# Performance work log

Measured on AMD Instinct MI355X. Metric: run time of the kernel, lower is better.

## Reference

```python
import jax, jax.numpy as jnp
import numpy as np

N_NODES = 100_000
N_EDGES = 1_600_000
F_DIM = 32


def setup_inputs() -> dict:
    key = jax.random.key(0)
    k1, k2, k3 = jax.random.split(key, 3)
    x = jax.random.normal(k1, (N_NODES, F_DIM), dtype=jnp.float32)
    edge_index = jax.random.randint(k2, (2, N_EDGES), 0, N_NODES, dtype=jnp.int64)
    edge_weight = jax.random.uniform(k3, (N_EDGES,), dtype=jnp.float32)
    w_mp = jnp.array([0.5], dtype=jnp.float32)  # learned scalar parameter
    return {"x": x, "edge_index": edge_index, "edge_weight": edge_weight, "w_mp": w_mp}


def reference(x, edge_index, edge_weight, w_mp):
    # message: ea = w_mp * x[src] * edge_weight  (shape [E, F])
    # aggregate: sum messages into target nodes (aggr='add', source_to_target)
    src = edge_index[0]
    dst = edge_index[1]
    ea = (w_mp * x[src]) * edge_weight[:, None]          # [E, F]
    out = jax.ops.segment_sum(ea, dst, num_segments=x.shape[0])  # [N, F]
    return out
```

## Files before the change

kernel.cpp:

```cpp
#include <hip/hip_runtime.h>


constexpr int N_NODES = 100000;
constexpr int N_EDGES = 1600000;
constexpr int F_DIM   = 32;

constexpr int NPB_C = 256;
constexpr int NB_C  = (N_NODES + NPB_C - 1) / NPB_C;
constexpr int CAP_C = 4608;

constexpr int CUR_STRIDE = 32;

constexpr int BIN_THREADS = 1024;
constexpr int BIN_BLOCKS  = 512;
constexpr int BIN_CHUNK   = N_EDGES / BIN_BLOCKS;
constexpr int BIN_EPT     = (BIN_CHUNK + BIN_THREADS - 1) / BIN_THREADS;

constexpr int AGG_THREADS = 1024;
constexpr int GRPT = (CAP_C + AGG_THREADS - 1) / AGG_THREADS;

constexpr size_t WS_CURSOR  = 0;
constexpr size_t WS_RECORDS = 64 * 1024;
constexpr size_t WS_NEEDED  = WS_RECORDS + (size_t)NB_C * CAP_C * 8;

__global__ __launch_bounds__(BIN_THREADS, 8) void bin_edges(
    const int* __restrict__ src, const int* __restrict__ dst,
    const float* __restrict__ ew, const float* __restrict__ w_mp,
    int* __restrict__ gcursor, uint2* __restrict__ records)
{
    __shared__ uint2 srt[BIN_CHUNK];
    __shared__ unsigned short srtb[BIN_CHUNK];
    __shared__ int lhist[NB_C];
    __shared__ int loff[NB_C];
    __shared__ int lbase[NB_C];
    __shared__ int lcur[NB_C];
    __shared__ int wsum[8];
    __shared__ int wexc[8];

    const int t    = threadIdx.x;
    const int lane = t & 63;
    const int wv   = t >> 6;

    if (t < NB_C) lhist[t] = 0;
    __syncthreads();

    const float w = w_mp[0];
    const int e0    = blockIdx.x * BIN_CHUNK;
    const int e_end = min(e0 + BIN_CHUNK, N_EDGES);
    const int cnt   = e_end - e0;

    int   bkt[BIN_EPT];
    uint2 rec[BIN_EPT];
    #pragma unroll
    for (int i = 0; i < BIN_EPT; ++i) {
        int j = t + i * BIN_THREADS;
        bkt[i] = -1;
        if (j < cnt) {
            int e = e0 + j;
            int d = dst[e];
            int b = d >> 8;
            bkt[i] = b;
            rec[i].x = __float_as_uint(w * ew[e]);
            rec[i].y = (unsigned)src[e] | ((unsigned)(d & 255) << 24);
            atomicAdd(&lhist[b], 1);
        }
    }
    __syncthreads();

    if (t < 448) {
        int v = (t < NB_C) ? lhist[t] : 0;
        int inc = v;
        #pragma unroll
        for (int d = 1; d < 64; d <<= 1) {
            int o = __shfl_up(inc, d, 64);
            if (lane >= d) inc += o;
        }
        if (lane == 63) wsum[wv] = inc;
        if (t < NB_C) loff[t] = inc - v;
    }
    __syncthreads();
    if (t < 64) {
        int v = (t < 7) ? wsum[t] : 0;
        int inc = v;
        #pragma unroll
        for (int d = 1; d < 8; d <<= 1) {
            int o = __shfl_up(inc, d, 64);
            if (t >= d) inc += o;
        }
        if (t < 7) wexc[t] = inc - v;
    }
    __syncthreads();

    if (t < NB_C) {
        int off = loff[t] + wexc[t >> 6];
        loff[t] = off;
        int c = lhist[t];
        int base = c ? atomicAdd(&gcursor[t * CUR_STRIDE], c) : 0;
        lbase[t] = t * CAP_C + base - off;
        lcur[t]  = off;
    }
    __syncthreads();

    #pragma unroll
    for (int i = 0; i < BIN_EPT; ++i) {
        if (bkt[i] >= 0) {
            int s = atomicAdd(&lcur[bkt[i]], 1);
            srt[s]  = rec[i];
            srtb[s] = (unsigned short)bkt[i];
        }
    }
    __syncthreads();

    for (int j = t; j < cnt; j += BIN_THREADS) {
        int b   = srtb[j];
        int pos = lbase[b] + j;
        if (pos < (b + 1) * CAP_C)
            records[pos] = srt[j];
    }
}

__global__ __launch_bounds__(AGG_THREADS, 8) void sort_gather(
    const int*   __restrict__ gcursor,
    const uint2* __restrict__ records,
    const float* __restrict__ x,
    float*       __restrict__ out)
{
    __shared__ uint2 sorted[CAP_C];
    __shared__ int   hist[NPB_C];
    __shared__ int   offs[NPB_C + 1];
    __shared__ int   cursor[NPB_C];

    const int coarse = blockIdx.x;
    const int t      = threadIdx.x;

    if (t < NPB_C) hist[t] = 0;
    __syncthreads();

    const int rbase = coarse * CAP_C;
    const int cnt   = min(gcursor[coarse * CUR_STRIDE], CAP_C);

    uint2 rec[GRPT];
    #pragma unroll
    for (int i = 0; i < GRPT; ++i) {
        int j = t + i * AGG_THREADS;
        rec[i].y = 0xFFFFFFFFu;
        if (j < cnt) {
            rec[i] = records[rbase + j];
            atomicAdd(&hist[rec[i].y >> 24], 1);
        }
    }
    __syncthreads();

    if (t < 64) {
        const int b4 = t * 4;
        int h0 = hist[b4], h1 = hist[b4 + 1], h2 = hist[b4 + 2], h3 = hist[b4 + 3];
        int s   = h0 + h1 + h2 + h3;
        int inc = s;
        #pragma unroll
        for (int d = 1; d < 64; d <<= 1) {
            int o = __shfl_up(inc, d, 64);
            if (t >= d) inc += o;
        }
        int base = inc - s;
        offs[b4]     = base;
        offs[b4 + 1] = base + h0;
        offs[b4 + 2] = base + h0 + h1;
        offs[b4 + 3] = base + h0 + h1 + h2;
        cursor[b4]     = base;
        cursor[b4 + 1] = base + h0;
        cursor[b4 + 2] = base + h0 + h1;
        cursor[b4 + 3] = base + h0 + h1 + h2;
        if (t == 63) offs[NPB_C] = inc;
    }
    __syncthreads();

    #pragma unroll
    for (int i = 0; i < GRPT; ++i) {
        if (rec[i].y != 0xFFFFFFFFu) {
            int slot = atomicAdd(&cursor[rec[i].y >> 24], 1);
            sorted[slot] = rec[i];
        }
    }
    __syncthreads();

    const int qq = (t & 7) * 4;
    #pragma unroll
    for (int p = 0; p < 2; ++p) {
        const int node  = p * (AGG_THREADS / 8) + (t >> 3);
        const int gnode = coarse * NPB_C + node;
        if (gnode >= N_NODES) continue;

        int j  = offs[node];
        int je = offs[node + 1];
        float4 acc = make_float4(0.f, 0.f, 0.f, 0.f);

        for (; j + 4 <= je; j += 4) {
            uint2 r0 = sorted[j + 0];
            uint2 r1 = sorted[j + 1];
            uint2 r2 = sorted[j + 2];
            uint2 r3 = sorted[j + 3];
            const float4 v0 = *reinterpret_cast<const float4*>(
                x + (size_t)(r0.y & 0xFFFFFFu) * F_DIM + qq);
            const float4 v1 = *reinterpret_cast<const float4*>(
                x + (size_t)(r1.y & 0xFFFFFFu) * F_DIM + qq);
            const float4 v2 = *reinterpret_cast<const float4*>(
                x + (size_t)(r2.y & 0xFFFFFFu) * F_DIM + qq);
            const float4 v3 = *reinterpret_cast<const float4*>(
                x + (size_t)(r3.y & 0xFFFFFFu) * F_DIM + qq);
            float c0 = __uint_as_float(r0.x), c1 = __uint_as_float(r1.x);
            float c2 = __uint_as_float(r2.x), c3 = __uint_as_float(r3.x);
            acc.x += c0 * v0.x + c1 * v1.x + c2 * v2.x + c3 * v3.x;
            acc.y += c0 * v0.y + c1 * v1.y + c2 * v2.y + c3 * v3.y;
            acc.z += c0 * v0.z + c1 * v1.z + c2 * v2.z + c3 * v3.z;
            acc.w += c0 * v0.w + c1 * v1.w + c2 * v2.w + c3 * v3.w;
        }
        for (; j < je; ++j) {
            uint2 r = sorted[j];
            float c = __uint_as_float(r.x);
            const float4 v = *reinterpret_cast<const float4*>(
                x + (size_t)(r.y & 0xFFFFFFu) * F_DIM + qq);
            acc.x += c * v.x;
            acc.y += c * v.y;
            acc.z += c * v.z;
            acc.w += c * v.w;
        }
        *reinterpret_cast<float4*>(out + (size_t)gnode * F_DIM + qq) = acc;
    }
}

__global__ __launch_bounds__(256) void gnn_scatter_atomic(
    const float* __restrict__ x, const int* __restrict__ src,
    const int* __restrict__ dst, const float* __restrict__ ew,
    const float* __restrict__ w_mp, float* __restrict__ out)
{
    const float w = w_mp[0];
    int gid = blockIdx.x * blockDim.x + threadIdx.x;
    int e = gid >> 3;
    int qq = (gid & 7) * 4;
    if (e >= N_EDGES) return;
    int s = src[e];
    int d = dst[e];
    float c = w * ew[e];
    const float4 xv = *reinterpret_cast<const float4*>(x + (size_t)s * F_DIM + qq);
    float* op = out + (size_t)d * F_DIM + qq;
    atomicAdd(op + 0, c * xv.x);
    atomicAdd(op + 1, c * xv.y);
    atomicAdd(op + 2, c * xv.z);
    atomicAdd(op + 3, c * xv.w);
}

extern "C" void kernel_launch(void* const* d_in, const int* in_sizes, int n_in,
                              void* d_out, int out_size, void* d_ws, size_t ws_size,
                              hipStream_t stream) {
    const float* x    = (const float*)d_in[0];
    const int*   ei   = (const int*)d_in[1];
    const float* ew   = (const float*)d_in[2];
    const float* w_mp = (const float*)d_in[3];
    float* out = (float*)d_out;

    const int* src = ei;
    const int* dst = ei + N_EDGES;

    if (ws_size < WS_NEEDED) {
        hipMemsetAsync(d_out, 0, (size_t)out_size * sizeof(float), stream);
        int total = N_EDGES * 8;
        gnn_scatter_atomic<<<(total + 255) / 256, 256, 0, stream>>>(
            x, src, dst, ew, w_mp, out);
        return;
    }

    char* ws = (char*)d_ws;
    int*   gcursor = (int*)(ws + WS_CURSOR);
    uint2* records = (uint2*)(ws + WS_RECORDS);

    hipMemsetAsync(gcursor, 0, NB_C * CUR_STRIDE * sizeof(int), stream);
    bin_edges<<<BIN_BLOCKS, BIN_THREADS, 0, stream>>>(src, dst, ew, w_mp,
                                                      gcursor, records);
    sort_gather<<<NB_C, AGG_THREADS, 0, stream>>>(gcursor, records, x, out);
}
```

Baseline: 122.4 us.

## Fuse binning and sort-gather into one persistent kernel with grid barrier

Merges the edge-binning kernel and the per-bucket sort/gather kernel into a single persistent kernel of 256 blocks. A software grid barrier on a global atomic counter separates the two phases, and shared memory is reused through a union. The aim is to remove one kernel launch and the idle gap between the kernels. In exchange, the number of blocks falls from 512 and 391 to 256, so each phase has less parallelism, and the barrier needs all 256 blocks to be co-resident or it can deadlock.

```diff
diff --git a/kernel.cpp b/kernel.cpp
--- a/kernel.cpp
+++ b/kernel.cpp
@@ -11,220 +11,236 @@
 
 constexpr int CUR_STRIDE = 32;
 
-constexpr int BIN_THREADS = 1024;
-constexpr int BIN_BLOCKS  = 512;
-constexpr int BIN_CHUNK   = N_EDGES / BIN_BLOCKS;
-constexpr int BIN_EPT     = (BIN_CHUNK + BIN_THREADS - 1) / BIN_THREADS;
-
-constexpr int AGG_THREADS = 1024;
-constexpr int GRPT = (CAP_C + AGG_THREADS - 1) / AGG_THREADS;
-
-constexpr size_t WS_CURSOR  = 0;
+constexpr int THREADS = 1024;
+constexpr int GRID    = 256;
+constexpr int NSUB    = 2;
+constexpr int SUBCH   = N_EDGES / (GRID * NSUB);
+constexpr int EPT     = (SUBCH + THREADS - 1) / THREADS;
+constexpr int GRPT    = (CAP_C + THREADS - 1) / THREADS;
+
+constexpr size_t WS_BAR     = 0;
+constexpr size_t WS_CURSOR  = 128;
 constexpr size_t WS_RECORDS = 64 * 1024;
 constexpr size_t WS_NEEDED  = WS_RECORDS + (size_t)NB_C * CAP_C * 8;
-
-__global__ __launch_bounds__(BIN_THREADS, 8) void bin_edges(
+constexpr size_t WS_ZERO    = 128 + (size_t)NB_C * CUR_STRIDE * 4;
+
+struct P1 {
+    uint2 srt[SUBCH];
+    unsigned short srtb[SUBCH];
+    int lhist[NB_C];
+    int loff[NB_C];
+    int lbase[NB_C];
+    int lcur[NB_C];
+    int wsum[8];
+    int wexc[8];
+};
+struct P2s {
+    uint2 sorted[CAP_C];
+    int hist[NPB_C];
+    int offs[NPB_C + 1];
+    int cursor[NPB_C];
+};
+union Smem { P1 p1; P2s p2; };
+
+__global__ __launch_bounds__(THREADS, 4) void fused_gnn(
     const int* __restrict__ src, const int* __restrict__ dst,
     const float* __restrict__ ew, const float* __restrict__ w_mp,
-    int* __restrict__ gcursor, uint2* __restrict__ records)
+    int* __restrict__ bar, int* __restrict__ gcursor,
+    uint2* __restrict__ records,
+    const float* __restrict__ x, float* __restrict__ out)
 {
-    __shared__ uint2 srt[BIN_CHUNK];
-    __shared__ unsigned short srtb[BIN_CHUNK];
-    __shared__ int lhist[NB_C];
-    __shared__ int loff[NB_C];
-    __shared__ int lbase[NB_C];
-    __shared__ int lcur[NB_C];
-    __shared__ int wsum[8];
-    __shared__ int wexc[8];
-
+    __shared__ Smem sm;
     const int t    = threadIdx.x;
     const int lane = t & 63;
     const int wv   = t >> 6;
-
-    if (t < NB_C) lhist[t] = 0;
+    const float w  = w_mp[0];
+
+    for (int sc = 0; sc < NSUB; ++sc) {
+        P1& p = sm.p1;
+        __syncthreads();
+        if (t < NB_C) p.lhist[t] = 0;
+        __syncthreads();
+
+        const int e0 = (blockIdx.x * NSUB + sc) * SUBCH;
+
+        int   bkt[EPT];
+        uint2 rec[EPT];
+        #pragma unroll
+        for (int i = 0; i < EPT; ++i) {
+            int j = t + i * THREADS;
+            bkt[i] = -1;
+            if (j < SUBCH) {
+                int e = e0 + j;
+                int d = dst[e];
+                int b = d >> 8;
+                bkt[i] = b;
+                rec[i].x = __float_as_uint(w * ew[e]);
+                rec[i].y = (unsigned)src[e] | ((unsigned)(d & 255) << 24);
+                atomicAdd(&p.lhist[b], 1);
+            }
+        }
+        __syncthreads();
+
+        if (t < 448) {
+            int v = (t < NB_C) ? p.lhist[t] : 0;
+            int inc = v;
+            #pragma unroll
+            for (int d = 1; d < 64; d <<= 1) {
+                int o = __shfl_up(inc, d, 64);
+                if (lane >= d) inc += o;
+            }
+            if (lane == 63) p.wsum[wv] = inc;
+            if (t < NB_C) p.loff[t] = inc - v;
+        }
+        __syncthreads();
+        if (t < 64) {
+            int v = (t < 7) ? p.wsum[t] : 0;
+            int inc = v;
+            #pragma unroll
+            for (int d = 1; d < 8; d <<= 1) {
+                int o = __shfl_up(inc, d, 64);
+                if (t >= d) inc += o;
+            }
+            if (t < 7) p.wexc[t] = inc - v;
+        }
+        __syncthreads();
+
+        if (t < NB_C) {
+            int off = p.loff[t] + p.wexc[t >> 6];
+            int c   = p.lhist[t];
+            int base = c ? atomicAdd(&gcursor[t * CUR_STRIDE], c) : 0;
+            p.lbase[t] = t * CAP_C + base - off;
+            p.lcur[t]  = off;
+        }
+        __syncthreads();
+
+        #pragma unroll
+        for (int i = 0; i < EPT; ++i) {
+            if (bkt[i] >= 0) {
+                int s = atomicAdd(&p.lcur[bkt[i]], 1);
+                p.srt[s]  = rec[i];
+                p.srtb[s] = (unsigned short)bkt[i];
+            }
+        }
+        __syncthreads();
+
+        for (int j = t; j < SUBCH; j += THREADS) {
+            int b   = p.srtb[j];
+            int pos = p.lbase[b] + j;
+            if (pos < (b + 1) * CAP_C)
+                records[pos] = p.srt[j];
+        }
+    }
+
+    __threadfence();
     __syncthreads();
-
-    const float w = w_mp[0];
-    const int e0    = blockIdx.x * BIN_CHUNK;
-    const int e_end = min(e0 + BIN_CHUNK, N_EDGES);
-    const int cnt   = e_end - e0;
-
-    int   bkt[BIN_EPT];
-    uint2 rec[BIN_EPT];
-    #pragma unroll
-    for (int i = 0; i < BIN_EPT; ++i) {
-        int j = t + i * BIN_THREADS;
-        bkt[i] = -1;
-        if (j < cnt) {
-            int e = e0 + j;
-            int d = dst[e];
-            int b = d >> 8;
-            bkt[i] = b;
-            rec[i].x = __float_as_uint(w * ew[e]);
-            rec[i].y = (unsigned)src[e] | ((unsigned)(d & 255) << 24);
-            atomicAdd(&lhist[b], 1);
-        }
+    if (t == 0) {
+        __hip_atomic_fetch_add(bar, 1, __ATOMIC_ACQ_REL,
+                               __HIP_MEMORY_SCOPE_AGENT);
+        while (__hip_atomic_load(bar, __ATOMIC_ACQUIRE,
+                                 __HIP_MEMORY_SCOPE_AGENT) < GRID)
+            __builtin_amdgcn_s_sleep(2);
     }
     __syncthreads();
-
-    if (t < 448) {
-        int v = (t < NB_C) ? lhist[t] : 0;
-        int inc = v;
-        #pragma unroll
-        for (int d = 1; d < 64; d <<= 1) {
-            int o = __shfl_up(inc, d, 64);
-            if (lane >= d) inc += o;
-        }
-        if (lane == 63) wsum[wv] = inc;
-        if (t < NB_C) loff[t] = inc - v;
-    }
-    __syncthreads();
-    if (t < 64) {
-        int v = (t < 7) ? wsum[t] : 0;
-        int inc = v;
-        #pragma unroll
-        for (int d = 1; d < 8; d <<= 1) {
-            int o = __shfl_up(inc, d, 64);
-            if (t >= d) inc += o;
-        }
-        if (t < 7) wexc[t] = inc - v;
-    }
-    __syncthreads();
-
-    if (t < NB_C) {
-        int off = loff[t] + wexc[t >> 6];
-        loff[t] = off;
-        int c = lhist[t];
-        int base = c ? atomicAdd(&gcursor[t * CUR_STRIDE], c) : 0;
-        lbase[t] = t * CAP_C + base - off;
-        lcur[t]  = off;
-    }
-    __syncthreads();
-
-    #pragma unroll
-    for (int i = 0; i < BIN_EPT; ++i) {
-        if (bkt[i] >= 0) {
-            int s = atomicAdd(&lcur[bkt[i]], 1);
-            srt[s]  = rec[i];
-            srtb[s] = (unsigned short)bkt[i];
-        }
-    }
-    __syncthreads();
-
-    for (int j = t; j < cnt; j += BIN_THREADS) {
-        int b   = srtb[j];
-        int pos = lbase[b] + j;
-        if (pos < (b + 1) * CAP_C)
-            records[pos] = srt[j];
-    }
-}
-
-__global__ __launch_bounds__(AGG_THREADS, 8) void sort_gather(
-    const int*   __restrict__ gcursor,
-    const uint2* __restrict__ records,
-    const float* __restrict__ x,
-    float*       __restrict__ out)
-{
-    __shared__ uint2 sorted[CAP_C];
-    __shared__ int   hist[NPB_C];
-    __shared__ int   offs[NPB_C + 1];
-    __shared__ int   cursor[NPB_C];
-
-    const int coarse = blockIdx.x;
-    const int t      = threadIdx.x;
-
-    if (t < NPB_C) hist[t] = 0;
-    __syncthreads();
-
-    const int rbase = coarse * CAP_C;
-    const int cnt   = min(gcursor[coarse * CUR_STRIDE], CAP_C);
-
-    uint2 rec[GRPT];
-    #pragma unroll
-    for (int i = 0; i < GRPT; ++i) {
-        int j = t + i * AGG_THREADS;
-        rec[i].y = 0xFFFFFFFFu;
-        if (j < cnt) {
-            rec[i] = records[rbase + j];
-            atomicAdd(&hist[rec[i].y >> 24], 1);
-        }
-    }
-    __syncthreads();
-
-    if (t < 64) {
-        const int b4 = t * 4;
-        int h0 = hist[b4], h1 = hist[b4 + 1], h2 = hist[b4 + 2], h3 = hist[b4 + 3];
-        int s   = h0 + h1 + h2 + h3;
-        int inc = s;
-        #pragma unroll
-        for (int d = 1; d < 64; d <<= 1) {
-            int o = __shfl_up(inc, d, 64);
-            if (t >= d) inc += o;
-        }
-        int base = inc - s;
-        offs[b4]     = base;
-        offs[b4 + 1] = base + h0;
-        offs[b4 + 2] = base + h0 + h1;
-        offs[b4 + 3] = base + h0 + h1 + h2;
-        cursor[b4]     = base;
-        cursor[b4 + 1] = base + h0;
-        cursor[b4 + 2] = base + h0 + h1;
-        cursor[b4 + 3] = base + h0 + h1 + h2;
-        if (t == 63) offs[NPB_C] = inc;
-    }
-    __syncthreads();
-
-    #pragma unroll
-    for (int i = 0; i < GRPT; ++i) {
-        if (rec[i].y != 0xFFFFFFFFu) {
-            int slot = atomicAdd(&cursor[rec[i].y >> 24], 1);
-            sorted[slot] = rec[i];
-        }
-    }
-    __syncthreads();
-
-    const int qq = (t & 7) * 4;
-    #pragma unroll
-    for (int p = 0; p < 2; ++p) {
-        const int node  = p * (AGG_THREADS / 8) + (t >> 3);
-        const int gnode = coarse * NPB_C + node;
-        if (gnode >= N_NODES) continue;
-
-        int j  = offs[node];
-        int je = offs[node + 1];
-        float4 acc = make_float4(0.f, 0.f, 0.f, 0.f);
-
-        for (; j + 4 <= je; j += 4) {
-            uint2 r0 = sorted[j + 0];
-            uint2 r1 = sorted[j + 1];
-            uint2 r2 = sorted[j + 2];
-            uint2 r3 = sorted[j + 3];
-            const float4 v0 = *reinterpret_cast<const float4*>(
-                x + (size_t)(r0.y & 0xFFFFFFu) * F_DIM + qq);
-            const float4 v1 = *reinterpret_cast<const float4*>(
-                x + (size_t)(r1.y & 0xFFFFFFu) * F_DIM + qq);
-            const float4 v2 = *reinterpret_cast<const float4*>(
-                x + (size_t)(r2.y & 0xFFFFFFu) * F_DIM + qq);
-            const float4 v3 = *reinterpret_cast<const float4*>(
-                x + (size_t)(r3.y & 0xFFFFFFu) * F_DIM + qq);
-            float c0 = __uint_as_float(r0.x), c1 = __uint_as_float(r1.x);
-            float c2 = __uint_as_float(r2.x), c3 = __uint_as_float(r3.x);
-            acc.x += c0 * v0.x + c1 * v1.x + c2 * v2.x + c3 * v3.x;
-            acc.y += c0 * v0.y + c1 * v1.y + c2 * v2.y + c3 * v3.y;
-            acc.z += c0 * v0.z + c1 * v1.z + c2 * v2.z + c3 * v3.z;
-            acc.w += c0 * v0.w + c1 * v1.w + c2 * v2.w + c3 * v3.w;
-        }
-        for (; j < je; ++j) {
-            uint2 r = sorted[j];
-            float c = __uint_as_float(r.x);
-            const float4 v = *reinterpret_cast<const float4*>(
-                x + (size_t)(r.y & 0xFFFFFFu) * F_DIM + qq);
-            acc.x += c * v.x;
-            acc.y += c * v.y;
-            acc.z += c * v.z;
-            acc.w += c * v.w;
-        }
-        *reinterpret_cast<float4*>(out + (size_t)gnode * F_DIM + qq) = acc;
+    __threadfence();
+
+    for (int k = blockIdx.x; k < NB_C; k += GRID) {
+        P2s& p = sm.p2;
+        __syncthreads();
+        if (t < NPB_C) p.hist[t] = 0;
+        __syncthreads();
+
+        const int rbase = k * CAP_C;
+        const int cnt   = min(gcursor[k * CUR_STRIDE], CAP_C);
+
+        uint2 rec[GRPT];
+        #pragma unroll
+        for (int i = 0; i < GRPT; ++i) {
+            int j = t + i * THREADS;
+            rec[i].y = 0xFFFFFFFFu;
+            if (j < cnt) {
+                rec[i] = records[rbase + j];
+                atomicAdd(&p.hist[rec[i].y >> 24], 1);
+            }
+        }
+        __syncthreads();
+
+        if (t < 64) {
+            const int b4 = t * 4;
+            int h0 = p.hist[b4], h1 = p.hist[b4 + 1];
+            int h2 = p.hist[b4 + 2], h3 = p.hist[b4 + 3];
+            int s   = h0 + h1 + h2 + h3;
+            int inc = s;
+            #pragma unroll
+            for (int d = 1; d < 64; d <<= 1) {
+                int o = __shfl_up(inc, d, 64);
+                if (t >= d) inc += o;
+            }
+            int base = inc - s;
+            p.offs[b4]     = base;
+            p.offs[b4 + 1] = base + h0;
+            p.offs[b4 + 2] = base + h0 + h1;
+            p.offs[b4 + 3] = base + h0 + h1 + h2;
+            p.cursor[b4]     = base;
+            p.cursor[b4 + 1] = base + h0;
+            p.cursor[b4 + 2] = base + h0 + h1;
+            p.cursor[b4 + 3] = base + h0 + h1 + h2;
+            if (t == 63) p.offs[NPB_C] = inc;
+        }
+        __syncthreads();
+
+        #pragma unroll
+        for (int i = 0; i < GRPT; ++i) {
+            if (rec[i].y != 0xFFFFFFFFu) {
+                int slot = atomicAdd(&p.cursor[rec[i].y >> 24], 1);
+                p.sorted[slot] = rec[i];
+            }
+        }
+        __syncthreads();
+
+        const int qq = (t & 7) * 4;
+        #pragma unroll
+        for (int ph = 0; ph < 2; ++ph) {
+            const int node  = ph * (THREADS / 8) + (t >> 3);
+            const int gnode = k * NPB_C + node;
+            if (gnode >= N_NODES) continue;
+
+            int j  = p.offs[node];
+            int je = p.offs[node + 1];
+            float4 acc = make_float4(0.f, 0.f, 0.f, 0.f);
+
+            for (; j + 4 <= je; j += 4) {
+                uint2 r0 = p.sorted[j + 0];
+                uint2 r1 = p.sorted[j + 1];
+                uint2 r2 = p.sorted[j + 2];
+                uint2 r3 = p.sorted[j + 3];
+                const float4 v0 = *reinterpret_cast<const float4*>(
+                    x + (size_t)(r0.y & 0xFFFFFFu) * F_DIM + qq);
+                const float4 v1 = *reinterpret_cast<const float4*>(
+                    x + (size_t)(r1.y & 0xFFFFFFu) * F_DIM + qq);
+                const float4 v2 = *reinterpret_cast<const float4*>(
+                    x + (size_t)(r2.y & 0xFFFFFFu) * F_DIM + qq);
+                const float4 v3 = *reinterpret_cast<const float4*>(
+                    x + (size_t)(r3.y & 0xFFFFFFu) * F_DIM + qq);
+                float c0 = __uint_as_float(r0.x), c1 = __uint_as_float(r1.x);
+                float c2 = __uint_as_float(r2.x), c3 = __uint_as_float(r3.x);
+                acc.x += c0 * v0.x + c1 * v1.x + c2 * v2.x + c3 * v3.x;
+                acc.y += c0 * v0.y + c1 * v1.y + c2 * v2.y + c3 * v3.y;
+                acc.z += c0 * v0.z + c1 * v1.z + c2 * v2.z + c3 * v3.z;
+                acc.w += c0 * v0.w + c1 * v1.w + c2 * v2.w + c3 * v3.w;
+            }
+            for (; j < je; ++j) {
+                uint2 r = p.sorted[j];
+                float c = __uint_as_float(r.x);
+                const float4 v = *reinterpret_cast<const float4*>(
+                    x + (size_t)(r.y & 0xFFFFFFu) * F_DIM + qq);
+                acc.x += c * v.x;
+                acc.y += c * v.y;
+                acc.z += c * v.z;
+                acc.w += c * v.w;
+            }
+            *reinterpret_cast<float4*>(out + (size_t)gnode * F_DIM + qq) = acc;
+        }
     }
 }
 
@@ -270,11 +286,11 @@
     }
 
     char* ws = (char*)d_ws;
+    int*   bar     = (int*)(ws + WS_BAR);
     int*   gcursor = (int*)(ws + WS_CURSOR);
     uint2* records = (uint2*)(ws + WS_RECORDS);
 
-    hipMemsetAsync(gcursor, 0, NB_C * CUR_STRIDE * sizeof(int), stream);
-    bin_edges<<<BIN_BLOCKS, BIN_THREADS, 0, stream>>>(src, dst, ew, w_mp,
-                                                      gcursor, records);
-    sort_gather<<<NB_C, AGG_THREADS, 0, stream>>>(gcursor, records, x, out);
+    hipMemsetAsync(ws, 0, WS_ZERO, stream);
+    fused_gnn<<<GRID, THREADS, 0, stream>>>(src, dst, ew, w_mp,
+                                            bar, gcursor, records, x, out);
 }
```

Result: slower. 313.3 us (+155.9%).
